# Kernel optimization log

Hardware: AMD Instinct MI355X
Metric: run time of the kernel (lower is better)

## Reference

```python
import jax, jax.numpy as jnp
import numpy as np

R = 65  # num_relations


def rgcn_conv(x, edge_index, edge_type, W, root, bias):
    """PyG RGCNConv with per-relation mean aggregation.
    Aggregate-then-transform (linearity lets us swap the order):
      mean_r[n] = mean over edges e with type r, dst(e)=n of x[src(e)]
      out = sum_r mean_r @ W_r + x @ root + bias
    """
    N = x.shape[0]
    src, dst = edge_index[0], edge_index[1]
    seg = edge_type * N + dst  # composite (relation, dst) segment id
    sums = jax.ops.segment_sum(x[src], seg, num_segments=R * N)
    sums = sums.reshape(R, N, -1)  # [R, N, F]
    cnt = jax.ops.segment_sum(jnp.ones(src.shape, x.dtype), seg, num_segments=R * N)
    cnt = cnt.reshape(R, N, 1)
    mean = sums / jnp.maximum(cnt, 1.0)
    return jnp.einsum('rni,rio->no', mean, W) + x @ root + bias


def setup_inputs() -> dict:
    key = jax.random.key(0)
    ks = jax.random.split(key, 20)
    N, E, F_in, H, M = 8000, 192000, 64, 256, 64
    B = 128
    inp = {
        'x': jax.random.normal(ks[0], (N, F_in), jnp.float32),
        'edge_index': jax.random.randint(ks[1], (2, E), 0, N),
        'edge_type': jax.random.randint(ks[2], (E,), 0, R),
        'batch': jnp.sort(jax.random.randint(ks[3], (N,), 0, B)),
    }
    def glorot(k, shape):
        fan = shape[-2] + shape[-1]
        return jax.random.normal(k, shape, jnp.float32) * jnp.sqrt(2.0 / fan)
    inp['W1'] = glorot(ks[4], (R, F_in, H)); inp['root1'] = glorot(ks[5], (F_in, H)); inp['b1'] = jnp.zeros((H,), jnp.float32)
    inp['W2'] = glorot(ks[6], (R, H, H));   inp['root2'] = glorot(ks[7], (H, H));   inp['b2'] = jnp.zeros((H,), jnp.float32)
    inp['W3'] = glorot(ks[8], (R, H, H));   inp['root3'] = glorot(ks[9], (H, H));   inp['b3'] = jnp.zeros((H,), jnp.float32)
    inp['ws_w'] = glorot(ks[10], (H, 1));    inp['ws_b'] = jnp.zeros((1,), jnp.float32)
    inp['m_w1'] = glorot(ks[11], (H, M)); inp['m_b1'] = jnp.zeros((M,), jnp.float32)
    inp['m_w2'] = glorot(ks[12], (M, M)); inp['m_b2'] = jnp.zeros((M,), jnp.float32)
    inp['m_w3'] = glorot(ks[13], (M, 1)); inp['m_b3'] = jnp.zeros((1,), jnp.float32)
    return inp


def reference(x, edge_index, edge_type, batch,
              W1, root1, b1, W2, root2, b2, W3, root3, b3,
              ws_w, ws_b, m_w1, m_b1, m_w2, m_b2, m_w3, m_b3):
    B = 128  # number of graphs in the batch
    h = jax.nn.relu(rgcn_conv(x, edge_index, edge_type, W1, root1, b1))
    h = jax.nn.relu(rgcn_conv(h, edge_index, edge_type, W2, root2, b2))
    h = jax.nn.relu(rgcn_conv(h, edge_index, edge_type, W3, root3, b3))
    # WeightedSum pooling: sigmoid gate per node, scatter-sum per graph
    w = jax.nn.sigmoid(h @ ws_w + ws_b)            # [N, 1]
    pooled = jax.ops.segment_sum(w * h, batch, num_segments=B)  # [B, H]
    # MLP head
    m = jax.nn.relu(pooled @ m_w1 + m_b1)
    m = jax.nn.relu(m @ m_w2 + m_b2)
    return m @ m_w3 + m_b3                          # [B, 1]
```

## Files before the change

### kernel.cpp

```cpp
#include <hip/hip_runtime.h>

#define NNODES 8000
#define NEDGES 192000
#define NREL   65
#define RP     66
#define HDIM   256
#define FDIM   64
#define NGRAPH 128
#define MDIM   64
#define TILE_M 64
#define MAXT   3456
#define EPTOT  (NEDGES + NNODES)

typedef _Float16 half8 __attribute__((ext_vector_type(8)));
typedef _Float16 half4 __attribute__((ext_vector_type(4)));
typedef float    f32x4 __attribute__((ext_vector_type(4)));
typedef unsigned int u32x4 __attribute__((ext_vector_type(4)));


__global__ void count_kernel(const int* __restrict__ ei, const int* __restrict__ et,
                             int* __restrict__ cnt_rn, int* __restrict__ type_cnt,
                             int* __restrict__ ddeg) {
    __shared__ int lbin[NREL];
    int tid = threadIdx.x;
    if (tid < NREL) lbin[tid] = 0;
    __syncthreads();
    int e = blockIdx.x * 256 + tid;
    if (e < NEDGES) {
        int t = et[e];
        int d = ei[NEDGES + e];
        atomicAdd(&lbin[t], 1);
        atomicAdd(&cnt_rn[t * NNODES + d], 1);
        atomicAdd(&ddeg[d], 1);
    }
    __syncthreads();
    if (tid < NREL && lbin[tid] > 0) atomicAdd(&type_cnt[tid], lbin[tid]);
}

__global__ void scan_tiles_kernel(const int* __restrict__ type_cnt, int* __restrict__ type_off,
                                  int* __restrict__ tile_rel, int* __restrict__ tile_start,
                                  int* __restrict__ tile_nrows) {
    __shared__ int s_off[RP + 1];
    __shared__ int s_toff[RP + 1];
    if (threadIdx.x == 0) {
        int off = 0, toff = 0;
        for (int r = 0; r < RP; r++) {
            int c = (r < NREL) ? type_cnt[r] : NNODES;
            s_off[r] = off; s_toff[r] = toff;
            off += c; toff += (c + TILE_M - 1) / TILE_M;
        }
        s_off[RP] = off; s_toff[RP] = toff;
        type_off[RP] = off;
    }
    __syncthreads();
    int r = threadIdx.x;
    if (r < RP) {
        type_off[r] = s_off[r];
        int c = s_off[r + 1] - s_off[r];
        int nt = (c + TILE_M - 1) / TILE_M;
        for (int i = 0; i < nt; i++) {
            int idx = s_toff[r] + i;
            tile_rel[idx]   = r;
            tile_start[idx] = s_off[r] + i * TILE_M;
            tile_nrows[idx] = min(TILE_M, c - i * TILE_M);
        }
    }
}

__global__ void dst_scan_kernel(const int* __restrict__ ddeg, int* __restrict__ dst_off) {
    __shared__ int part[256];
    int t = threadIdx.x;
    int base = t * 32;
    int s = 0;
    for (int i = 0; i < 32; i++) {
        int n = base + i;
        if (n < NNODES) s += ddeg[n] + 1;
    }
    part[t] = s;
    __syncthreads();
    if (t == 0) {
        int run = 0;
        for (int i = 0; i < 256; i++) { int tmp = part[i]; part[i] = run; run += tmp; }
        dst_off[NNODES] = run;
    }
    __syncthreads();
    int run = part[t];
    for (int i = 0; i < 32; i++) {
        int n = base + i;
        if (n < NNODES) { dst_off[n] = run; run += ddeg[n] + 1; }
    }
}

__global__ void scatter_kernel(const int* __restrict__ ei, const int* __restrict__ et,
                               const int* __restrict__ cnt_rn, const int* __restrict__ type_off,
                               int* __restrict__ type_cur,
                               const int* __restrict__ dst_off, int* __restrict__ dst_cur,
                               int* __restrict__ esrc, int* __restrict__ eq,
                               float* __restrict__ escale) {
    __shared__ int lbin[NREL];
    __shared__ int gbase[NREL];
    int tid = threadIdx.x;
    if (tid < NREL) lbin[tid] = 0;
    __syncthreads();
    int i = blockIdx.x * 256 + tid;
    int t = 0, lrank = 0;
    bool is_edge = (i < NEDGES);
    if (is_edge) {
        t = et[i];
        lrank = atomicAdd(&lbin[t], 1);
    }
    __syncthreads();
    if (tid < NREL && lbin[tid] > 0) gbase[tid] = atomicAdd(&type_cur[tid], lbin[tid]);
    __syncthreads();
    if (is_edge) {
        int d = ei[NEDGES + i];
        int p = type_off[t] + gbase[t] + lrank;
        int q = dst_off[d] + atomicAdd(&dst_cur[d], 1);
        esrc[p] = ei[i];
        eq[p] = q;
        escale[p] = 1.0f / (float)cnt_rn[t * NNODES + d];
    } else if (i < EPTOT) {
        int n = i - NEDGES;
        int p = NEDGES + n;
        int q = dst_off[n] + atomicAdd(&dst_cur[n], 1);
        esrc[p] = n; eq[p] = q; escale[p] = 1.0f;
    }
}

__global__ void convW_kernel(const float* __restrict__ W, const float* __restrict__ root,
                             _Float16* __restrict__ Wt, int K) {
    int r = blockIdx.x, k0 = blockIdx.y * 32, n0 = blockIdx.z * 32;
    const float* src = (r < NREL) ? (W + (size_t)r * K * HDIM) : root;
    __shared__ float tile[32][33];
    int tj = threadIdx.x & 31, ti = threadIdx.x >> 5;
    #pragma unroll
    for (int s = 0; s < 4; s++) {
        int i = ti + s * 8;
        tile[i][tj] = src[(size_t)(k0 + i) * HDIM + n0 + tj];
    }
    __syncthreads();
    #pragma unroll
    for (int s = 0; s < 4; s++) {
        int i = ti + s * 8;
        Wt[((size_t)r * HDIM + (n0 + i)) * K + k0 + tj] = (_Float16)tile[tj][i];
    }
}

__global__ void conv_x_kernel(const float* __restrict__ x, _Float16* __restrict__ x16) {
    int i = blockIdx.x * 256 + threadIdx.x;
    if (i < NNODES * FDIM) x16[i] = (_Float16)x[i];
}

template <int K>
__global__ __launch_bounds__(256, 8)
void edge_gemm_kernel(const _Float16* __restrict__ hin, const _Float16* __restrict__ Wt,
                      const int* __restrict__ esrc, const int* __restrict__ eq,
                      const float* __restrict__ escale,
                      const int* __restrict__ tile_rel, const int* __restrict__ tile_start,
                      const int* __restrict__ tile_nrows,
                      _Float16* __restrict__ Y) {
    int bid = blockIdx.x;
    int ch  = (bid >= MAXT) ? 1 : 0;
    int t   = bid - ch * MAXT;
    int x = t & 7, i = t >> 3;
    int c = i / 48, j = i % 48;
    int tile = c * 384 + x * 48 + j;

    int nr = tile_nrows[tile];
    if (nr == 0) return;
    int r  = tile_rel[tile];
    int ts = tile_start[tile];

    constexpr int KH  = (K > 128) ? 128 : K;
    constexpr int LK  = KH + 8;
    constexpr int SO  = 136;
    constexpr int AEL = TILE_M * LK;
    constexpr int OEL = TILE_M * SO;
    constexpr int EL  = (AEL > OEL) ? AEL : OEL;
    __shared__ _Float16 sbuf[EL];
    __shared__ int   sq[TILE_M];
    __shared__ float sscale[TILE_M];

    int tid = threadIdx.x;
    if (tid < TILE_M) {
        if (tid < nr) { sq[tid] = eq[ts + tid]; sscale[tid] = escale[ts + tid]; }
        else          { sq[tid] = 0;            sscale[tid] = 0.f; }
    }

    int lane = tid & 63, w = tid >> 6;
    int lm = lane & 15, quad = lane >> 4;
    f32x4 acc[4][2] = {};
    const _Float16* Bbase = Wt + ((size_t)r * HDIM + ch * 128 + w * 32 + lm) * K + quad * 8;
    const _Float16* Abase = sbuf + lm * LK + quad * 8;

    constexpr int CPR = KH / 8;
    for (int kh = 0; kh < K; kh += KH) {
        for (int idx = tid; idx < TILE_M * CPR; idx += 256) {
            int row = idx / CPR, cc = idx % CPR;
            u32x4 v = {0, 0, 0, 0};
            if (row < nr) {
                int src = esrc[ts + row];
                v = *(const u32x4*)(hin + (size_t)src * K + kh + cc * 8);
            }
            *(u32x4*)&sbuf[row * LK + cc * 8] = v;
        }
        __syncthreads();

        for (int kk = 0; kk < KH; kk += 32) {
            half8 b0 = *(const half8*)(Bbase + kh + kk);
            half8 b1 = *(const half8*)(Bbase + 16 * K + kh + kk);
            #pragma unroll
            for (int mt = 0; mt < 4; mt++) {
                half8 a = *(const half8*)(Abase + mt * 16 * LK + kk);
                acc[mt][0] = __builtin_amdgcn_mfma_f32_16x16x32_f16(a, b0, acc[mt][0], 0, 0, 0);
                acc[mt][1] = __builtin_amdgcn_mfma_f32_16x16x32_f16(a, b1, acc[mt][1], 0, 0, 0);
            }
        }
        __syncthreads();
    }

    #pragma unroll
    for (int mt = 0; mt < 4; mt++) {
        #pragma unroll
        for (int rr = 0; rr < 4; rr++) {
            int row = mt * 16 + quad * 4 + rr;
            float s = sscale[row];
            #pragma unroll
            for (int nt = 0; nt < 2; nt++)
                sbuf[row * SO + w * 32 + nt * 16 + lm] = (_Float16)(acc[mt][nt][rr] * s);
        }
    }
    __syncthreads();
    for (int idx = tid; idx < TILE_M * 16; idx += 256) {
        int row = idx >> 4, seg = idx & 15;
        if (row < nr) {
            u32x4 v = *(const u32x4*)&sbuf[row * SO + seg * 8];
            __builtin_nontemporal_store(v, (u32x4*)(Y + (size_t)sq[row] * HDIM + ch * 128 + seg * 8));
        }
    }
}

__global__ __launch_bounds__(256)
void reduce_kernel(const _Float16* __restrict__ Y, const int* __restrict__ dst_off,
                   const float* __restrict__ bias, _Float16* __restrict__ hout) {
    int node = blockIdx.x * 4 + (threadIdx.x >> 6);
    int lane = threadIdx.x & 63;
    int start = dst_off[node], end = dst_off[node + 1];
    int c = lane & 31;
    int r = lane >> 5;
    float acc[8] = {0, 0, 0, 0, 0, 0, 0, 0};
    for (int jj = start + r; jj < end; jj += 2) {
        u32x4 u = __builtin_nontemporal_load((const u32x4*)(Y + (size_t)jj * HDIM + c * 8));
        half8 v = *(half8*)&u;
        #pragma unroll
        for (int k = 0; k < 8; k++) acc[k] += (float)v[k];
    }
    #pragma unroll
    for (int k = 0; k < 8; k++) acc[k] += __shfl_down(acc[k], 32, 64);
    if (lane < 32) {
        half8 o;
        #pragma unroll
        for (int k = 0; k < 8; k++) {
            float v = acc[k] + bias[c * 8 + k];
            o[k] = (_Float16)(v > 0.f ? v : 0.f);
        }
        *(half8*)(hout + (size_t)node * HDIM + c * 8) = o;
    }
}


__global__ void gate_kernel(const _Float16* __restrict__ h, const float* __restrict__ ws_w,
                            const float* __restrict__ ws_b, float* __restrict__ gate) {
    int node = blockIdx.x * 4 + (threadIdx.x >> 6);
    int lane = threadIdx.x & 63;
    half4 v = *(const half4*)(h + (size_t)node * HDIM + lane * 4);
    float s = 0.f;
    #pragma unroll
    for (int k = 0; k < 4; k++) s += (float)v[k] * ws_w[lane * 4 + k];
    for (int o = 32; o > 0; o >>= 1) s += __shfl_down(s, o, 64);
    if (lane == 0) gate[node] = 1.f / (1.f + __expf(-(s + ws_b[0])));
}

__global__ void pool_kernel(const _Float16* __restrict__ h, const float* __restrict__ gate,
                            const int* __restrict__ batch, float* __restrict__ pooled) {
    int g = blockIdx.x, t = threadIdx.x;
    int a = 0, b = NNODES;
    while (a < b) { int m = (a + b) >> 1; if (batch[m] < g) a = m + 1; else b = m; }
    int lo = a;
    b = NNODES;
    while (a < b) { int m = (a + b) >> 1; if (batch[m] < g + 1) a = m + 1; else b = m; }
    int hi = a;
    float acc = 0.f;
    for (int n = lo; n < hi; n++)
        acc += gate[n] * (float)h[(size_t)n * HDIM + t];
    pooled[(size_t)g * HDIM + t] = acc;
}

__global__ void head_kernel(const float* __restrict__ pooled,
                            const float* __restrict__ w1, const float* __restrict__ b1,
                            const float* __restrict__ w2, const float* __restrict__ b2,
                            const float* __restrict__ w3, const float* __restrict__ b3,
                            float* __restrict__ out) {
    int b = blockIdx.x, tid = threadIdx.x;
    __shared__ float sp[HDIM];
    __shared__ float m1[MDIM];
    __shared__ float m2[MDIM];
    for (int i = tid; i < HDIM; i += 64) sp[i] = pooled[(size_t)b * HDIM + i];
    __syncthreads();
    float a = b1[tid];
    for (int i = 0; i < HDIM; i++) a += sp[i] * w1[i * MDIM + tid];
    m1[tid] = a > 0.f ? a : 0.f;
    __syncthreads();
    float c = b2[tid];
    for (int i = 0; i < MDIM; i++) c += m1[i] * w2[i * MDIM + tid];
    m2[tid] = c > 0.f ? c : 0.f;
    __syncthreads();
    float p = m2[tid] * w3[tid];
    for (int o = 32; o > 0; o >>= 1) p += __shfl_down(p, o, 64);
    if (tid == 0) out[b] = p + b3[0];
}


extern "C" void kernel_launch(void* const* d_in, const int* in_sizes, int n_in,
                              void* d_out, int out_size, void* d_ws, size_t ws_size,
                              hipStream_t stream) {
    const float* x     = (const float*)d_in[0];
    const int*   ei    = (const int*)d_in[1];
    const int*   et    = (const int*)d_in[2];
    const int*   batch = (const int*)d_in[3];
    const float* W1    = (const float*)d_in[4];
    const float* root1 = (const float*)d_in[5];
    const float* b1    = (const float*)d_in[6];
    const float* W2    = (const float*)d_in[7];
    const float* root2 = (const float*)d_in[8];
    const float* b2    = (const float*)d_in[9];
    const float* W3    = (const float*)d_in[10];
    const float* root3 = (const float*)d_in[11];
    const float* b3    = (const float*)d_in[12];
    const float* ws_w  = (const float*)d_in[13];
    const float* ws_b  = (const float*)d_in[14];
    const float* m_w1  = (const float*)d_in[15];
    const float* m_b1  = (const float*)d_in[16];
    const float* m_w2  = (const float*)d_in[17];
    const float* m_b2  = (const float*)d_in[18];
    const float* m_w3  = (const float*)d_in[19];
    const float* m_b3  = (const float*)d_in[20];
    float* out = (float*)d_out;

    char* ws = (char*)d_ws;
    size_t o = 0;
    auto take = [&](size_t bytes) { size_t r = o; o = (o + bytes + 255) & ~(size_t)255; return r; };

    size_t o_cnt_rn = take((size_t)NREL * NNODES * 4);
    size_t o_tcnt   = take(RP * 4);
    size_t o_tcur   = take(RP * 4);
    size_t o_toff   = take((RP + 1) * 4);
    size_t o_ddeg   = take((size_t)NNODES * 4);
    size_t o_dcur   = take((size_t)NNODES * 4);
    size_t o_doff   = take((size_t)(NNODES + 1) * 4);
    size_t o_esrc   = take((size_t)EPTOT * 4);
    size_t o_eq     = take((size_t)EPTOT * 4);
    size_t o_escale = take((size_t)EPTOT * 4);
    size_t o_trel   = take(MAXT * 4);
    size_t o_tstart = take(MAXT * 4);
    size_t o_tnrows = take(MAXT * 4);
    size_t o_wt1    = take((size_t)RP * HDIM * FDIM * 2);
    size_t o_wt2    = take((size_t)RP * HDIM * HDIM * 2);
    size_t o_wt3    = take((size_t)RP * HDIM * HDIM * 2);
    size_t o_x16    = take((size_t)NNODES * FDIM * 2);
    size_t o_h16    = take((size_t)NNODES * HDIM * 2);
    size_t o_gate   = take((size_t)NNODES * 4);
    size_t o_pool   = take((size_t)NGRAPH * HDIM * 4);
    size_t o_y16    = take((size_t)EPTOT * HDIM * 2);

    int*      cnt_rn   = (int*)(ws + o_cnt_rn);
    int*      type_cnt = (int*)(ws + o_tcnt);
    int*      type_cur = (int*)(ws + o_tcur);
    int*      type_off = (int*)(ws + o_toff);
    int*      ddeg     = (int*)(ws + o_ddeg);
    int*      dst_cur  = (int*)(ws + o_dcur);
    int*      dst_off  = (int*)(ws + o_doff);
    int*      esrc     = (int*)(ws + o_esrc);
    int*      eq       = (int*)(ws + o_eq);
    float*    escale   = (float*)(ws + o_escale);
    int*      trel     = (int*)(ws + o_trel);
    int*      tstart   = (int*)(ws + o_tstart);
    int*      tnrows   = (int*)(ws + o_tnrows);
    _Float16* Wt1      = (_Float16*)(ws + o_wt1);
    _Float16* Wt2      = (_Float16*)(ws + o_wt2);
    _Float16* Wt3      = (_Float16*)(ws + o_wt3);
    _Float16* x16      = (_Float16*)(ws + o_x16);
    _Float16* h16      = (_Float16*)(ws + o_h16);
    float*    gate     = (float*)(ws + o_gate);
    float*    pooled   = (float*)(ws + o_pool);
    _Float16* Y16      = (_Float16*)(ws + o_y16);

    hipMemsetAsync(ws + o_cnt_rn, 0, o_toff - o_cnt_rn, stream);
    hipMemsetAsync(ws + o_ddeg, 0, o_doff - o_ddeg, stream);
    hipMemsetAsync(ws + o_tnrows, 0, MAXT * 4, stream);

    count_kernel<<<(NEDGES + 255) / 256, 256, 0, stream>>>(ei, et, cnt_rn, type_cnt, ddeg);
    scan_tiles_kernel<<<1, 128, 0, stream>>>(type_cnt, type_off, trel, tstart, tnrows);
    dst_scan_kernel<<<1, 256, 0, stream>>>(ddeg, dst_off);
    scatter_kernel<<<(EPTOT + 255) / 256, 256, 0, stream>>>(ei, et, cnt_rn, type_off, type_cur,
                                                            dst_off, dst_cur, esrc, eq, escale);

    convW_kernel<<<dim3(RP, FDIM / 32, HDIM / 32), 256, 0, stream>>>(W1, root1, Wt1, FDIM);
    convW_kernel<<<dim3(RP, HDIM / 32, HDIM / 32), 256, 0, stream>>>(W2, root2, Wt2, HDIM);
    convW_kernel<<<dim3(RP, HDIM / 32, HDIM / 32), 256, 0, stream>>>(W3, root3, Wt3, HDIM);
    conv_x_kernel<<<(NNODES * FDIM + 255) / 256, 256, 0, stream>>>(x, x16);

    edge_gemm_kernel<FDIM><<<2 * MAXT, 256, 0, stream>>>(x16, Wt1, esrc, eq, escale,
                                                         trel, tstart, tnrows, Y16);
    reduce_kernel<<<NNODES / 4, 256, 0, stream>>>(Y16, dst_off, b1, h16);

    edge_gemm_kernel<HDIM><<<2 * MAXT, 256, 0, stream>>>(h16, Wt2, esrc, eq, escale,
                                                         trel, tstart, tnrows, Y16);
    reduce_kernel<<<NNODES / 4, 256, 0, stream>>>(Y16, dst_off, b2, h16);

    edge_gemm_kernel<HDIM><<<2 * MAXT, 256, 0, stream>>>(h16, Wt3, esrc, eq, escale,
                                                         trel, tstart, tnrows, Y16);
    reduce_kernel<<<NNODES / 4, 256, 0, stream>>>(Y16, dst_off, b3, h16);

    gate_kernel<<<NNODES / 4, 256, 0, stream>>>(h16, ws_w, ws_b, gate);
    pool_kernel<<<NGRAPH, 256, 0, stream>>>(h16, gate, batch, pooled);
    head_kernel<<<NGRAPH, 64, 0, stream>>>(pooled, m_w1, m_b1, m_w2, m_b2, m_w3, m_b3, out);

    (void)in_sizes; (void)n_in; (void)out_size; (void)ws_size;
}
```

Baseline: 511.3 us.

## Split edge GEMM tiles by row halves instead of output column halves

The edge GEMM kernel now gives each block 32 edge rows and all 256 output columns, instead of 64 rows and half of the columns. The gathered source features are loaded once per row rather than twice (once per column half), and partially filled tiles can skip the empty second row half. The cost is that each block now reads the full relation weight slice (twice as many B fragments per wave), and the output staging buffer is wider.

```diff
diff --git a/kernel.cpp b/kernel.cpp
--- a/kernel.cpp
+++ b/kernel.cpp
@@ -160,45 +160,47 @@
                       const int* __restrict__ tile_nrows,
                       _Float16* __restrict__ Y) {
     int bid = blockIdx.x;
-    int ch  = (bid >= MAXT) ? 1 : 0;
-    int t   = bid - ch * MAXT;
+    int rh  = (bid >= MAXT) ? 1 : 0;
+    int t   = bid - rh * MAXT;
     int x = t & 7, i = t >> 3;
     int c = i / 48, j = i % 48;
     int tile = c * 384 + x * 48 + j;
 
     int nr = tile_nrows[tile];
-    if (nr == 0) return;
-    int r  = tile_rel[tile];
-    int ts = tile_start[tile];
+    int r0 = rh * 32;
+    if (nr <= r0) return;
+    int nloc = min(32, nr - r0);
+    int rel  = tile_rel[tile];
+    int ts   = tile_start[tile] + r0;
 
     constexpr int KH  = (K > 128) ? 128 : K;
     constexpr int LK  = KH + 8;
-    constexpr int SO  = 136;
-    constexpr int AEL = TILE_M * LK;
-    constexpr int OEL = TILE_M * SO;
+    constexpr int SO  = HDIM + 8;
+    constexpr int AEL = 32 * LK;
+    constexpr int OEL = 32 * SO;
     constexpr int EL  = (AEL > OEL) ? AEL : OEL;
     __shared__ _Float16 sbuf[EL];
-    __shared__ int   sq[TILE_M];
-    __shared__ float sscale[TILE_M];
+    __shared__ int   sq[32];
+    __shared__ float sscale[32];
 
     int tid = threadIdx.x;
-    if (tid < TILE_M) {
-        if (tid < nr) { sq[tid] = eq[ts + tid]; sscale[tid] = escale[ts + tid]; }
-        else          { sq[tid] = 0;            sscale[tid] = 0.f; }
+    if (tid < 32) {
+        if (tid < nloc) { sq[tid] = eq[ts + tid]; sscale[tid] = escale[ts + tid]; }
+        else            { sq[tid] = 0;            sscale[tid] = 0.f; }
     }
 
     int lane = tid & 63, w = tid >> 6;
     int lm = lane & 15, quad = lane >> 4;
-    f32x4 acc[4][2] = {};
-    const _Float16* Bbase = Wt + ((size_t)r * HDIM + ch * 128 + w * 32 + lm) * K + quad * 8;
+    f32x4 acc[2][4] = {};
+    const _Float16* Bbase = Wt + ((size_t)rel * HDIM + w * 64 + lm) * K + quad * 8;
     const _Float16* Abase = sbuf + lm * LK + quad * 8;
 
     constexpr int CPR = KH / 8;
     for (int kh = 0; kh < K; kh += KH) {
-        for (int idx = tid; idx < TILE_M * CPR; idx += 256) {
+        for (int idx = tid; idx < 32 * CPR; idx += 256) {
             int row = idx / CPR, cc = idx % CPR;
             u32x4 v = {0, 0, 0, 0};
-            if (row < nr) {
+            if (row < nloc) {
                 int src = esrc[ts + row];
                 v = *(const u32x4*)(hin + (size_t)src * K + kh + cc * 8);
             }
@@ -207,35 +209,35 @@
         __syncthreads();
 
         for (int kk = 0; kk < KH; kk += 32) {
-            half8 b0 = *(const half8*)(Bbase + kh + kk);
-            half8 b1 = *(const half8*)(Bbase + 16 * K + kh + kk);
+            half8 a0 = *(const half8*)(Abase + kk);
+            half8 a1 = *(const half8*)(Abase + 16 * LK + kk);
             #pragma unroll
-            for (int mt = 0; mt < 4; mt++) {
-                half8 a = *(const half8*)(Abase + mt * 16 * LK + kk);
-                acc[mt][0] = __builtin_amdgcn_mfma_f32_16x16x32_f16(a, b0, acc[mt][0], 0, 0, 0);
-                acc[mt][1] = __builtin_amdgcn_mfma_f32_16x16x32_f16(a, b1, acc[mt][1], 0, 0, 0);
+            for (int nt = 0; nt < 4; nt++) {
+                half8 b = *(const half8*)(Bbase + nt * 16 * K + kh + kk);
+                acc[0][nt] = __builtin_amdgcn_mfma_f32_16x16x32_f16(a0, b, acc[0][nt], 0, 0, 0);
+                acc[1][nt] = __builtin_amdgcn_mfma_f32_16x16x32_f16(a1, b, acc[1][nt], 0, 0, 0);
             }
         }
         __syncthreads();
     }
 
     #pragma unroll
-    for (int mt = 0; mt < 4; mt++) {
+    for (int mt = 0; mt < 2; mt++) {
         #pragma unroll
         for (int rr = 0; rr < 4; rr++) {
             int row = mt * 16 + quad * 4 + rr;
             float s = sscale[row];
             #pragma unroll
-            for (int nt = 0; nt < 2; nt++)
-                sbuf[row * SO + w * 32 + nt * 16 + lm] = (_Float16)(acc[mt][nt][rr] * s);
-        }
-    }
-    __syncthreads();
-    for (int idx = tid; idx < TILE_M * 16; idx += 256) {
-        int row = idx >> 4, seg = idx & 15;
-        if (row < nr) {
+            for (int nt = 0; nt < 4; nt++)
+                sbuf[row * SO + w * 64 + nt * 16 + lm] = (_Float16)(acc[mt][nt][rr] * s);
+        }
+    }
+    __syncthreads();
+    for (int idx = tid; idx < 32 * 32; idx += 256) {
+        int row = idx >> 5, seg = idx & 31;
+        if (row < nloc) {
             u32x4 v = *(const u32x4*)&sbuf[row * SO + seg * 8];
-            __builtin_nontemporal_store(v, (u32x4*)(Y + (size_t)sq[row] * HDIM + ch * 128 + seg * 8));
+            __builtin_nontemporal_store(v, (u32x4*)(Y + (size_t)sq[row] * HDIM + seg * 8));
         }
     }
 }
```

New measurement: 596.1 us. 16.6% more time.

## Process two tiles per block with full 256-column output and register-staged prefetch

Applied to the files above, without the earlier changes.

Each block in the edge GEMM now handles a pair of tiles and computes all 256 output columns, where before each block did half the columns of one tile. The gathered source rows are loaded into registers while the previous chunk's MFMAs run, then written to LDS, so gather latency overlaps compute. The larger 4x4 MFMA accumulator per wave raises reuse of each A and B fragment and avoids gathering the same rows twice, but register pressure rises and launch bounds drop to 3 blocks per SIMD, lowering occupancy. The grid shrinks to MAXT/2 blocks.

```diff
diff --git a/kernel.cpp b/kernel.cpp
--- a/kernel.cpp
+++ b/kernel.cpp
@@ -10,6 +10,7 @@
 #define MDIM   64
 #define TILE_M 64
 #define MAXT   3456
+#define NPAIR  (MAXT / 2)
 #define EPTOT  (NEDGES + NNODES)
 
 typedef _Float16 half8 __attribute__((ext_vector_type(8)));
@@ -152,91 +153,146 @@
 }
 
 template <int K>
-__global__ __launch_bounds__(256, 8)
+__global__ __launch_bounds__(256, 3)
 void edge_gemm_kernel(const _Float16* __restrict__ hin, const _Float16* __restrict__ Wt,
                       const int* __restrict__ esrc, const int* __restrict__ eq,
                       const float* __restrict__ escale,
                       const int* __restrict__ tile_rel, const int* __restrict__ tile_start,
                       const int* __restrict__ tile_nrows,
                       _Float16* __restrict__ Y) {
-    int bid = blockIdx.x;
-    int ch  = (bid >= MAXT) ? 1 : 0;
-    int t   = bid - ch * MAXT;
-    int x = t & 7, i = t >> 3;
-    int c = i / 48, j = i % 48;
-    int tile = c * 384 + x * 48 + j;
-
-    int nr = tile_nrows[tile];
-    if (nr == 0) return;
-    int r  = tile_rel[tile];
-    int ts = tile_start[tile];
-
-    constexpr int KH  = (K > 128) ? 128 : K;
-    constexpr int LK  = KH + 8;
-    constexpr int SO  = 136;
-    constexpr int AEL = TILE_M * LK;
-    constexpr int OEL = TILE_M * SO;
-    constexpr int EL  = (AEL > OEL) ? AEL : OEL;
-    __shared__ _Float16 sbuf[EL];
-    __shared__ int   sq[TILE_M];
-    __shared__ float sscale[TILE_M];
+    constexpr int KH   = (K > 128) ? 128 : K;
+    constexpr int LK   = KH + 8;
+    constexpr int SO   = HDIM + 8;
+    constexpr int CPR  = KH / 8;
+    constexpr int CPT  = (TILE_M * CPR) / 256;
+    constexpr int RSTEP = 256 / CPR;
+
+    __shared__ _Float16 abuf[TILE_M * LK];
+    __shared__ _Float16 obuf[TILE_M * SO];
+
+    int p = blockIdx.x;
+    int x = p & 7, ii = p >> 3;
+    int pc = ii / 24, pj = ii % 24;
+    int pair = pc * 192 + x * 24 + pj;
+    int t0 = pair * 2, t1 = t0 + 1;
+
+    int nr0 = tile_nrows[t0], nr1 = tile_nrows[t1];
+    if ((nr0 | nr1) == 0) return;
+    int ts0 = tile_start[t0], ts1 = tile_start[t1];
+    int rel0 = tile_rel[t0],  rel1 = tile_rel[t1];
 
     int tid = threadIdx.x;
-    if (tid < TILE_M) {
-        if (tid < nr) { sq[tid] = eq[ts + tid]; sscale[tid] = escale[ts + tid]; }
-        else          { sq[tid] = 0;            sscale[tid] = 0.f; }
-    }
-
     int lane = tid & 63, w = tid >> 6;
     int lm = lane & 15, quad = lane >> 4;
-    f32x4 acc[4][2] = {};
-    const _Float16* Bbase = Wt + ((size_t)r * HDIM + ch * 128 + w * 32 + lm) * K + quad * 8;
-    const _Float16* Abase = sbuf + lm * LK + quad * 8;
-
-    constexpr int CPR = KH / 8;
-    for (int kh = 0; kh < K; kh += KH) {
-        for (int idx = tid; idx < TILE_M * CPR; idx += 256) {
-            int row = idx / CPR, cc = idx % CPR;
+
+    int ch   = tid % CPR;
+    int row0 = tid / CPR;
+
+    u32x4 sreg[CPT];
+    f32x4 acc[4][4] = {};
+
+    auto LOADR = [&](int nr, int ts, int kh) {
+        #pragma unroll
+        for (int q = 0; q < CPT; q++) {
+            int row = row0 + q * RSTEP;
             u32x4 v = {0, 0, 0, 0};
             if (row < nr) {
                 int src = esrc[ts + row];
-                v = *(const u32x4*)(hin + (size_t)src * K + kh + cc * 8);
+                v = *(const u32x4*)(hin + (size_t)src * K + kh + ch * 8);
             }
-            *(u32x4*)&sbuf[row * LK + cc * 8] = v;
-        }
-        __syncthreads();
-
+            sreg[q] = v;
+        }
+    };
+    auto DSW = [&]() {
+        #pragma unroll
+        for (int q = 0; q < CPT; q++) {
+            int row = row0 + q * RSTEP;
+            *(u32x4*)&abuf[row * LK + ch * 8] = sreg[q];
+        }
+    };
+    auto MFMA = [&](int rel, int kh) {
+        const _Float16* Bb = Wt + ((size_t)rel * HDIM + w * 64 + lm) * K + kh + quad * 8;
+        const _Float16* Ab = abuf + lm * LK + quad * 8;
         for (int kk = 0; kk < KH; kk += 32) {
-            half8 b0 = *(const half8*)(Bbase + kh + kk);
-            half8 b1 = *(const half8*)(Bbase + 16 * K + kh + kk);
+            half8 a[4], b[4];
             #pragma unroll
-            for (int mt = 0; mt < 4; mt++) {
-                half8 a = *(const half8*)(Abase + mt * 16 * LK + kk);
-                acc[mt][0] = __builtin_amdgcn_mfma_f32_16x16x32_f16(a, b0, acc[mt][0], 0, 0, 0);
-                acc[mt][1] = __builtin_amdgcn_mfma_f32_16x16x32_f16(a, b1, acc[mt][1], 0, 0, 0);
+            for (int mt = 0; mt < 4; mt++) a[mt] = *(const half8*)(Ab + mt * 16 * LK + kk);
+            #pragma unroll
+            for (int nt = 0; nt < 4; nt++) b[nt] = *(const half8*)(Bb + (size_t)nt * 16 * K + kk);
+            #pragma unroll
+            for (int mt = 0; mt < 4; mt++)
+                #pragma unroll
+                for (int nt = 0; nt < 4; nt++)
+                    acc[mt][nt] = __builtin_amdgcn_mfma_f32_16x16x32_f16(a[mt], b[nt], acc[mt][nt], 0, 0, 0);
+        }
+    };
+    auto EPI_LDS = [&](int nr, int ts) {
+        #pragma unroll
+        for (int mt = 0; mt < 4; mt++) {
+            #pragma unroll
+            for (int rr = 0; rr < 4; rr++) {
+                int row = mt * 16 + quad * 4 + rr;
+                float s = (row < nr) ? escale[ts + row] : 0.f;
+                #pragma unroll
+                for (int nt = 0; nt < 4; nt++)
+                    obuf[row * SO + w * 64 + nt * 16 + lm] = (_Float16)(acc[mt][nt][rr] * s);
             }
         }
-        __syncthreads();
-    }
-
-    #pragma unroll
-    for (int mt = 0; mt < 4; mt++) {
-        #pragma unroll
-        for (int rr = 0; rr < 4; rr++) {
-            int row = mt * 16 + quad * 4 + rr;
-            float s = sscale[row];
+    };
+    auto EPI_STORE = [&](int nr, int ts) {
+        for (int idx = tid; idx < TILE_M * 32; idx += 256) {
+            int row = idx >> 5, seg = idx & 31;
+            if (row < nr) {
+                int qq = eq[ts + row];
+                u32x4 v = *(const u32x4*)&obuf[row * SO + seg * 8];
+                __builtin_nontemporal_store(v, (u32x4*)(Y + (size_t)qq * HDIM + seg * 8));
+            }
+        }
+    };
+    auto ZACC = [&]() {
+        #pragma unroll
+        for (int mt = 0; mt < 4; mt++)
             #pragma unroll
-            for (int nt = 0; nt < 2; nt++)
-                sbuf[row * SO + w * 32 + nt * 16 + lm] = (_Float16)(acc[mt][nt][rr] * s);
-        }
-    }
-    __syncthreads();
-    for (int idx = tid; idx < TILE_M * 16; idx += 256) {
-        int row = idx >> 4, seg = idx & 15;
-        if (row < nr) {
-            u32x4 v = *(const u32x4*)&sbuf[row * SO + seg * 8];
-            __builtin_nontemporal_store(v, (u32x4*)(Y + (size_t)sq[row] * HDIM + ch * 128 + seg * 8));
-        }
+            for (int nt = 0; nt < 4; nt++)
+                acc[mt][nt] = f32x4{0.f, 0.f, 0.f, 0.f};
+    };
+
+    if constexpr (K > 128) {
+        LOADR(nr0, ts0, 0);  DSW();  __syncthreads();
+        LOADR(nr0, ts0, KH);
+        MFMA(rel0, 0);
+        __syncthreads();
+        DSW();  __syncthreads();
+        LOADR(nr1, ts1, 0);
+        MFMA(rel0, KH);
+        EPI_LDS(nr0, ts0);
+        __syncthreads();
+        EPI_STORE(nr0, ts0);
+        DSW();
+        __syncthreads();
+        ZACC();
+        LOADR(nr1, ts1, KH);
+        MFMA(rel1, 0);
+        __syncthreads();
+        DSW();  __syncthreads();
+        MFMA(rel1, KH);
+        EPI_LDS(nr1, ts1);
+        __syncthreads();
+        EPI_STORE(nr1, ts1);
+    } else {
+        LOADR(nr0, ts0, 0);  DSW();  __syncthreads();
+        LOADR(nr1, ts1, 0);
+        MFMA(rel0, 0);
+        EPI_LDS(nr0, ts0);
+        __syncthreads();
+        EPI_STORE(nr0, ts0);
+        DSW();
+        __syncthreads();
+        ZACC();
+        MFMA(rel1, 0);
+        EPI_LDS(nr1, ts1);
+        __syncthreads();
+        EPI_STORE(nr1, ts1);
     }
 }
 
@@ -410,16 +466,16 @@
     convW_kernel<<<dim3(RP, HDIM / 32, HDIM / 32), 256, 0, stream>>>(W3, root3, Wt3, HDIM);
     conv_x_kernel<<<(NNODES * FDIM + 255) / 256, 256, 0, stream>>>(x, x16);
 
-    edge_gemm_kernel<FDIM><<<2 * MAXT, 256, 0, stream>>>(x16, Wt1, esrc, eq, escale,
-                                                         trel, tstart, tnrows, Y16);
+    edge_gemm_kernel<FDIM><<<NPAIR, 256, 0, stream>>>(x16, Wt1, esrc, eq, escale,
+                                                      trel, tstart, tnrows, Y16);
     reduce_kernel<<<NNODES / 4, 256, 0, stream>>>(Y16, dst_off, b1, h16);
 
-    edge_gemm_kernel<HDIM><<<2 * MAXT, 256, 0, stream>>>(h16, Wt2, esrc, eq, escale,
-                                                         trel, tstart, tnrows, Y16);
+    edge_gemm_kernel<HDIM><<<NPAIR, 256, 0, stream>>>(h16, Wt2, esrc, eq, escale,
+                                                      trel, tstart, tnrows, Y16);
     reduce_kernel<<<NNODES / 4, 256, 0, stream>>>(Y16, dst_off, b2, h16);
 
-    edge_gemm_kernel<HDIM><<<2 * MAXT, 256, 0, stream>>>(h16, Wt3, esrc, eq, escale,
-                                                         trel, tstart, tnrows, Y16);
+    edge_gemm_kernel<HDIM><<<NPAIR, 256, 0, stream>>>(h16, Wt3, esrc, eq, escale,
+                                                      trel, tstart, tnrows, Y16);
     reduce_kernel<<<NNODES / 4, 256, 0, stream>>>(Y16, dst_off, b3, h16);
 
     gate_kernel<<<NNODES / 4, 256, 0, stream>>>(h16, ws_w, ws_b, gate);
```

Measured after the change: 565.0 us. +10.5%, slower.

## Compute full 256-wide output per edge tile with direct-to-LDS swizzled gather

Applied to the files above, without the earlier changes.

Each block now computes all 256 output columns for its 64-edge tile instead of splitting the columns across two blocks, so each gathered source row is loaded once rather than twice. The gather uses global_load_lds with an XOR swizzle to fill shared memory directly, and the whole K dimension is staged at once. It also removes the occupancy hint and simplifies the tile-to-block mapping. The cost is larger shared memory per block (about 33KB at K=256), 64 accumulator registers per thread and half as many blocks, which may lower occupancy and latency hiding.

```diff
diff --git a/kernel.cpp b/kernel.cpp
--- a/kernel.cpp
+++ b/kernel.cpp
@@ -152,29 +152,23 @@
 }
 
 template <int K>
-__global__ __launch_bounds__(256, 8)
+__global__ __launch_bounds__(256)
 void edge_gemm_kernel(const _Float16* __restrict__ hin, const _Float16* __restrict__ Wt,
                       const int* __restrict__ esrc, const int* __restrict__ eq,
                       const float* __restrict__ escale,
                       const int* __restrict__ tile_rel, const int* __restrict__ tile_start,
                       const int* __restrict__ tile_nrows,
                       _Float16* __restrict__ Y) {
-    int bid = blockIdx.x;
-    int ch  = (bid >= MAXT) ? 1 : 0;
-    int t   = bid - ch * MAXT;
-    int x = t & 7, i = t >> 3;
-    int c = i / 48, j = i % 48;
-    int tile = c * 384 + x * 48 + j;
+    int bid  = blockIdx.x;
+    int tile = (bid & 7) * (MAXT / 8) + (bid >> 3);
 
     int nr = tile_nrows[tile];
     if (nr == 0) return;
     int r  = tile_rel[tile];
     int ts = tile_start[tile];
 
-    constexpr int KH  = (K > 128) ? 128 : K;
-    constexpr int LK  = KH + 8;
-    constexpr int SO  = 136;
-    constexpr int AEL = TILE_M * LK;
+    constexpr int SO  = HDIM + 8;
+    constexpr int AEL = TILE_M * K;
     constexpr int OEL = TILE_M * SO;
     constexpr int EL  = (AEL > OEL) ? AEL : OEL;
     __shared__ _Float16 sbuf[EL];
@@ -182,42 +176,52 @@
     __shared__ float sscale[TILE_M];
 
     int tid = threadIdx.x;
+    int lane = tid & 63, w = tid >> 6;
+    int lm = lane & 15, quad = lane >> 4;
+
+    constexpr int CPR = K / 8;
+    constexpr int IPW = (TILE_M * CPR) / 256;
+    int rl = lane / CPR;
+    int cs = lane % CPR;
+    #pragma unroll
+    for (int i = 0; i < IPW; i++) {
+        int rr  = (w * IPW + i) * (64 / CPR) + rl;
+        int src = esrc[ts + ((rr < nr) ? rr : 0)];
+        int c   = cs ^ (rr & 7);
+        const _Float16* gp = hin + (size_t)src * K + c * 8;
+        _Float16* lp = sbuf + (w * IPW + i) * 512;
+        __builtin_amdgcn_global_load_lds(
+            (const __attribute__((address_space(1))) void*)gp,
+            (__attribute__((address_space(3))) void*)lp,
+            16, 0, 0);
+    }
     if (tid < TILE_M) {
         if (tid < nr) { sq[tid] = eq[ts + tid]; sscale[tid] = escale[ts + tid]; }
         else          { sq[tid] = 0;            sscale[tid] = 0.f; }
     }
-
-    int lane = tid & 63, w = tid >> 6;
-    int lm = lane & 15, quad = lane >> 4;
-    f32x4 acc[4][2] = {};
-    const _Float16* Bbase = Wt + ((size_t)r * HDIM + ch * 128 + w * 32 + lm) * K + quad * 8;
-    const _Float16* Abase = sbuf + lm * LK + quad * 8;
-
-    constexpr int CPR = KH / 8;
-    for (int kh = 0; kh < K; kh += KH) {
-        for (int idx = tid; idx < TILE_M * CPR; idx += 256) {
-            int row = idx / CPR, cc = idx % CPR;
-            u32x4 v = {0, 0, 0, 0};
-            if (row < nr) {
-                int src = esrc[ts + row];
-                v = *(const u32x4*)(hin + (size_t)src * K + kh + cc * 8);
-            }
-            *(u32x4*)&sbuf[row * LK + cc * 8] = v;
-        }
-        __syncthreads();
-
-        for (int kk = 0; kk < KH; kk += 32) {
-            half8 b0 = *(const half8*)(Bbase + kh + kk);
-            half8 b1 = *(const half8*)(Bbase + 16 * K + kh + kk);
+    __syncthreads();
+
+    f32x4 acc[4][4] = {};
+    const _Float16* Bbase = Wt + ((size_t)r * HDIM + w * 64 + lm) * K + quad * 8;
+    int axor = lm & 7;
+
+    for (int kk = 0; kk < K; kk += 32) {
+        half8 a[4], b[4];
+        int cidx = (((kk >> 3) + quad) ^ axor) * 8;
+        #pragma unroll
+        for (int mt = 0; mt < 4; mt++)
+            a[mt] = *(const half8*)(sbuf + (mt * 16 + lm) * K + cidx);
+        #pragma unroll
+        for (int nt = 0; nt < 4; nt++)
+            b[nt] = *(const half8*)(Bbase + nt * 16 * K + kk);
+        #pragma unroll
+        for (int mt = 0; mt < 4; mt++)
             #pragma unroll
-            for (int mt = 0; mt < 4; mt++) {
-                half8 a = *(const half8*)(Abase + mt * 16 * LK + kk);
-                acc[mt][0] = __builtin_amdgcn_mfma_f32_16x16x32_f16(a, b0, acc[mt][0], 0, 0, 0);
-                acc[mt][1] = __builtin_amdgcn_mfma_f32_16x16x32_f16(a, b1, acc[mt][1], 0, 0, 0);
-            }
-        }
-        __syncthreads();
-    }
+            for (int nt = 0; nt < 4; nt++)
+                acc[mt][nt] = __builtin_amdgcn_mfma_f32_16x16x32_f16(a[mt], b[nt], acc[mt][nt], 0, 0, 0);
+    }
+
+    __syncthreads();
 
     #pragma unroll
     for (int mt = 0; mt < 4; mt++) {
@@ -226,16 +230,17 @@
             int row = mt * 16 + quad * 4 + rr;
             float s = sscale[row];
             #pragma unroll
-            for (int nt = 0; nt < 2; nt++)
-                sbuf[row * SO + w * 32 + nt * 16 + lm] = (_Float16)(acc[mt][nt][rr] * s);
+            for (int nt = 0; nt < 4; nt++)
+                sbuf[row * SO + w * 64 + nt * 16 + lm] = (_Float16)(acc[mt][nt][rr] * s);
         }
     }
     __syncthreads();
-    for (int idx = tid; idx < TILE_M * 16; idx += 256) {
-        int row = idx >> 4, seg = idx & 15;
+
+    for (int idx = tid; idx < TILE_M * 32; idx += 256) {
+        int row = idx >> 5, seg = idx & 31;
         if (row < nr) {
             u32x4 v = *(const u32x4*)&sbuf[row * SO + seg * 8];
-            __builtin_nontemporal_store(v, (u32x4*)(Y + (size_t)sq[row] * HDIM + ch * 128 + seg * 8));
+            __builtin_nontemporal_store(v, (u32x4*)(Y + (size_t)sq[row] * HDIM + seg * 8));
         }
     }
 }
@@ -410,16 +415,16 @@
     convW_kernel<<<dim3(RP, HDIM / 32, HDIM / 32), 256, 0, stream>>>(W3, root3, Wt3, HDIM);
     conv_x_kernel<<<(NNODES * FDIM + 255) / 256, 256, 0, stream>>>(x, x16);
 
-    edge_gemm_kernel<FDIM><<<2 * MAXT, 256, 0, stream>>>(x16, Wt1, esrc, eq, escale,
-                                                         trel, tstart, tnrows, Y16);
+    edge_gemm_kernel<FDIM><<<MAXT, 256, 0, stream>>>(x16, Wt1, esrc, eq, escale,
+                                                     trel, tstart, tnrows, Y16);
     reduce_kernel<<<NNODES / 4, 256, 0, stream>>>(Y16, dst_off, b1, h16);
 
-    edge_gemm_kernel<HDIM><<<2 * MAXT, 256, 0, stream>>>(h16, Wt2, esrc, eq, escale,
-                                                         trel, tstart, tnrows, Y16);
+    edge_gemm_kernel<HDIM><<<MAXT, 256, 0, stream>>>(h16, Wt2, esrc, eq, escale,
+                                                     trel, tstart, tnrows, Y16);
     reduce_kernel<<<NNODES / 4, 256, 0, stream>>>(Y16, dst_off, b2, h16);
 
-    edge_gemm_kernel<HDIM><<<2 * MAXT, 256, 0, stream>>>(h16, Wt3, esrc, eq, escale,
-                                                         trel, tstart, tnrows, Y16);
+    edge_gemm_kernel<HDIM><<<MAXT, 256, 0, stream>>>(h16, Wt3, esrc, eq, escale,
+                                                     trel, tstart, tnrows, Y16);
     reduce_kernel<<<NNODES / 4, 256, 0, stream>>>(Y16, dst_off, b3, h16);
 
     gate_kernel<<<NNODES / 4, 256, 0, stream>>>(h16, ws_w, ws_b, gate);
```

New measurement: 483.0 us. 1.06x faster.
